# Kernel optimization log

Hardware: AMD Instinct MI355X
Metric: run time of the kernel (lower is better)

## Reference

```python
import jax, jax.numpy as jnp
import numpy as np
import math

B, S, E, H = 4, 1024, 1024, 16
D = E // H


def setup_inputs() -> dict:
    key = jax.random.key(0)
    ks = jax.random.split(key, 10)
    inp = {
        "query": jax.random.normal(ks[0], (B, S, E), dtype=jnp.float32),
        "key": jax.random.normal(ks[1], (B, S, E), dtype=jnp.float32),
        "value": jax.random.normal(ks[2], (B, S, E), dtype=jnp.float32),
        "attn_mask": jax.random.randint(ks[3], (B * H, S, S), 0, 2).astype(bool),
        "key_padding_mask": jax.random.randint(ks[4], (B, S), 0, 2).astype(bool),
        # nn.Linear(E, E, bias=False) weights, stored [out, in] as in torch
        "Wq": jax.random.normal(ks[5], (E, E), dtype=jnp.float32) * 0.02,
        "Wk": jax.random.normal(ks[6], (E, E), dtype=jnp.float32) * 0.02,
        "Wv": jax.random.normal(ks[7], (E, E), dtype=jnp.float32) * 0.02,
        "Wo": jax.random.normal(ks[8], (E, E), dtype=jnp.float32) * 0.02,
    }
    return inp


def reference(query, key, value, attn_mask, key_padding_mask, Wq, Wk, Wv, Wo):
    # projections: torch Linear => x @ W.T; split heads -> [B,H,S,D]
    Q = (query @ Wq.T).reshape(B, S, H, D).transpose(0, 2, 1, 3)
    K = (key @ Wk.T).reshape(B, S, H, D).transpose(0, 2, 1, 3)
    V = (value @ Wv.T).reshape(B, S, H, D).transpose(0, 2, 1, 3)

    scores = jnp.einsum('bhid,bhkd->bhik', Q, K) / math.sqrt(D)  # [B,H,S,S]

    am = attn_mask.reshape(B, H, S, S)
    kpm = jnp.broadcast_to(key_padding_mask[:, None, None, :], (B, H, S, S))
    mask = am | kpm

    # faithful quirks: masked scores set to 0 (not -inf); softmax over dim=2
    # (the QUERY axis i of [b,h,i,k]); masked weights zeroed after softmax.
    scores = jnp.where(mask, 0.0, scores)
    weights = jax.nn.softmax(scores, axis=2)
    weights = jnp.where(mask, 0.0, weights)

    attn = jnp.einsum('bhij,bhjk->bhik', weights, V)  # [B,H,S,D]
    attn = attn.transpose(0, 2, 1, 3).reshape(B, S, H * D)
    return attn @ Wo.T
```

## Files before the change

kernel.cpp:

```cpp
#include <hip/hip_runtime.h>
#include <stdint.h>

#define S_ 1024
#define E_ 1024
#define H_ 16
#define D_ 64
#define BH_ 64

typedef __attribute__((ext_vector_type(4))) float f32x4;
typedef __attribute__((ext_vector_type(8))) _Float16 f16x8;

__device__ __forceinline__ void gl_lds16(const void* g, void* l) {
  __builtin_amdgcn_global_load_lds((__attribute__((address_space(1))) void*)(g),
                                   (__attribute__((address_space(3))) void*)(l), 16, 0, 0);
}

__global__ __launch_bounds__(256) void cvt_f16(const float* __restrict__ q,
                                               const float* __restrict__ k,
                                               const float* __restrict__ v,
                                               const float* __restrict__ wq,
                                               const float* __restrict__ wk,
                                               const float* __restrict__ wv,
                                               const float* __restrict__ wo,
                                               _Float16* __restrict__ dst) {
  size_t i = ((size_t)blockIdx.x * 256 + threadIdx.x) * 4;
  const size_t M4 = 4u << 20, M1 = 1u << 20;
  const float* src;
  size_t off;
  if (i < M4) { src = q; off = i; }
  else if (i < 2 * M4) { src = k; off = i - M4; }
  else if (i < 3 * M4) { src = v; off = i - 2 * M4; }
  else if (i < 3 * M4 + M1) { src = wq; off = i - 3 * M4; }
  else if (i < 3 * M4 + 2 * M1) { src = wk; off = i - (3 * M4 + M1); }
  else if (i < 3 * M4 + 3 * M1) { src = wv; off = i - (3 * M4 + 2 * M1); }
  else { src = wo; off = i - (3 * M4 + 3 * M1); }
  float4 f = *reinterpret_cast<const float4*>(src + off);
  _Float16 h[4];
  h[0] = (_Float16)f.x; h[1] = (_Float16)f.y; h[2] = (_Float16)f.z; h[3] = (_Float16)f.w;
  *reinterpret_cast<uint2*>(dst + i) = *reinterpret_cast<uint2*>(h);
}

__global__ __launch_bounds__(256) void pack_mask(const int* __restrict__ am,
                                                 const int* __restrict__ kpm,
                                                 uint32_t* __restrict__ mw) {
  size_t t = (size_t)blockIdx.x * 256 + threadIdx.x;
  size_t f = t * 4;
  int k = (int)(f & (S_ - 1));
  int b = (int)(f >> 24);
  int4 a = *reinterpret_cast<const int4*>(am + f);
  int4 kp = *reinterpret_cast<const int4*>(kpm + (size_t)b * S_ + k);
  uint32_t nib = (uint32_t)((a.x | kp.x) != 0) | ((uint32_t)((a.y | kp.y) != 0) << 1) |
                 ((uint32_t)((a.z | kp.z) != 0) << 2) | ((uint32_t)((a.w | kp.w) != 0) << 3);
  uint32_t v = nib << ((threadIdx.x & 7) * 4);
  v |= __shfl_xor(v, 1);
  v |= __shfl_xor(v, 2);
  v |= __shfl_xor(v, 4);
  if ((threadIdx.x & 7) == 0) mw[t >> 3] = v;
}

__global__ __launch_bounds__(256) void gemm_proj(const _Float16* __restrict__ qkv,
                                                 const _Float16* __restrict__ wts,
                                                 _Float16* __restrict__ QKo,
                                                 _Float16* __restrict__ Vt) {
  const int K = 1024, BM = 128, BK = 32;
  __shared__ __align__(16) _Float16 As[BM * BK];
  __shared__ __align__(16) _Float16 Bs[BM * BK];
  const int tid = threadIdx.x, wave = tid >> 6, lane = tid & 63;
  const int l15 = lane & 15, lk = lane >> 4;
  const int wr = wave >> 1, wc = wave & 1;
  const int mb = blockIdx.x, nb = blockIdx.y, z = blockIdx.z;
  const _Float16* A = qkv + (size_t)z * (4u << 20);
  const _Float16* Bw = wts + (size_t)z * (1u << 20);
  const int srow = (lane >> 2);
  const int scol = (lane & 3) * 8;
  f32x4 acc[4][4] = {};
  for (int kt = 0; kt < K / BK; ++kt) {
#pragma unroll
    for (int c = 0; c < 2; ++c) {
      int ch = wave * 2 + c;
      int row = ch * 16 + srow;
      gl_lds16(&A[(size_t)(mb * BM + row) * K + kt * BK + scol], &As[ch * 512]);
      gl_lds16(&Bw[(size_t)(nb * BM + row) * K + kt * BK + scol], &Bs[ch * 512]);
    }
    __syncthreads();
    f16x8 a[4], b[4];
#pragma unroll
    for (int m = 0; m < 4; ++m)
      a[m] = *reinterpret_cast<const f16x8*>(&As[(wr * 64 + m * 16 + l15) * BK + lk * 8]);
#pragma unroll
    for (int n = 0; n < 4; ++n)
      b[n] = *reinterpret_cast<const f16x8*>(&Bs[(wc * 64 + n * 16 + l15) * BK + lk * 8]);
#pragma unroll
    for (int m = 0; m < 4; ++m)
#pragma unroll
      for (int n = 0; n < 4; ++n)
        acc[m][n] = __builtin_amdgcn_mfma_f32_16x16x32_f16(a[m], b[n], acc[m][n], 0, 0, 0);
    __syncthreads();
  }
  const float qs = (z == 0) ? 0.125f : 1.0f;
#pragma unroll
  for (int m = 0; m < 4; ++m) {
#pragma unroll
    for (int n = 0; n < 4; ++n) {
#pragma unroll
      for (int r = 0; r < 4; ++r) {
        int gm = mb * BM + wr * 64 + m * 16 + lk * 4 + r;
        int gn = nb * BM + wc * 64 + n * 16 + l15;
        int bb = gm >> 10, s = gm & 1023, h = gn >> 6, d = gn & 63;
        int bh = bb * 16 + h;
        _Float16 v = (_Float16)(acc[m][n][r] * qs);
        if (z == 2)
          Vt[((size_t)bh * D_ + d) * S_ + s] = v;
        else
          QKo[(size_t)z * (4u << 20) + ((size_t)bh * S_ + s) * D_ + d] = v;
      }
    }
  }
}

__global__ __launch_bounds__(256) void attn_pass_a(const _Float16* __restrict__ Qh,
                                                   const _Float16* __restrict__ Kh,
                                                   const uint32_t* __restrict__ mw,
                                                   float* __restrict__ denom,
                                                   _Float16* __restrict__ Wg) {
  const int TI = 128, TK = 128, LD = 72, LW = 144;
  __shared__ __align__(16) _Float16 Qs[TI * LD];
  __shared__ __align__(16) _Float16 Ks[TK * LD];
  __shared__ __align__(16) _Float16 Ws[TI * LW];
  __shared__ uint32_t Ms[TI * 4];
  __shared__ float red[4][64];
  const int tid = threadIdx.x, wave = tid >> 6, lane = tid & 63;
  const int l15 = lane & 15, lk = lane >> 4;
  const int wr = wave >> 1, wc = wave & 1;
  const int bh = blockIdx.y, kb = blockIdx.x;
  const _Float16* Qb = Qh + (size_t)bh * S_ * D_;
  const _Float16* Kb = Kh + (size_t)bh * S_ * D_;
  const uint32_t* mrow = mw + (size_t)bh * S_ * 32;
#pragma unroll
  for (int j = 0; j < 4; ++j) {
    int c = tid + j * 256;
    int row = c >> 3, c8 = c & 7;
    *reinterpret_cast<uint4*>(&Ks[row * LD + c8 * 8]) =
        *reinterpret_cast<const uint4*>(&Kb[(size_t)(kb * TK + row) * D_ + c8 * 8]);
  }
  float csum[4] = {0.f, 0.f, 0.f, 0.f};
  for (int ib = 0; ib < S_ / TI; ++ib) {
    __syncthreads();
#pragma unroll
    for (int j = 0; j < 4; ++j) {
      int c = tid + j * 256;
      int row = c >> 3, c8 = c & 7;
      *reinterpret_cast<uint4*>(&Qs[row * LD + c8 * 8]) =
          *reinterpret_cast<const uint4*>(&Qb[(size_t)(ib * TI + row) * D_ + c8 * 8]);
    }
    Ms[tid] = mrow[(size_t)(ib * TI + (tid >> 2)) * 32 + kb * 4 + (tid & 3)];
    Ms[tid + 256] = mrow[(size_t)(ib * TI + 64 + (tid >> 2)) * 32 + kb * 4 + (tid & 3)];
    __syncthreads();
    f32x4 acc[4][4] = {};
#pragma unroll
    for (int kk = 0; kk < 2; ++kk) {
      f16x8 a[4], b[4];
#pragma unroll
      for (int m = 0; m < 4; ++m)
        a[m] = *reinterpret_cast<const f16x8*>(&Qs[(wr * 64 + m * 16 + l15) * LD + kk * 32 + lk * 8]);
#pragma unroll
      for (int n = 0; n < 4; ++n)
        b[n] = *reinterpret_cast<const f16x8*>(&Ks[(wc * 64 + n * 16 + l15) * LD + kk * 32 + lk * 8]);
#pragma unroll
      for (int m = 0; m < 4; ++m)
#pragma unroll
        for (int n = 0; n < 4; ++n)
          acc[m][n] = __builtin_amdgcn_mfma_f32_16x16x32_f16(a[m], b[n], acc[m][n], 0, 0, 0);
    }
#pragma unroll
    for (int n = 0; n < 4; ++n) {
      int kcol = wc * 64 + n * 16 + l15;
      int kwl = kcol >> 5;
      int kbit = kcol & 31;
      float part = 0.f;
#pragma unroll
      for (int m = 0; m < 4; ++m) {
        int lr0 = wr * 64 + m * 16 + lk * 4;
#pragma unroll
        for (int r = 0; r < 4; ++r) {
          bool msk = (Ms[(lr0 + r) * 4 + kwl] >> kbit) & 1;
          float e = __expf(acc[m][n][r]);
          part += msk ? 1.0f : e;
          Ws[(lr0 + r) * LW + kcol] = msk ? (_Float16)0.f : (_Float16)e;
        }
      }
      csum[n] += part;
    }
    __syncthreads();
#pragma unroll
    for (int j = 0; j < 8; ++j) {
      int c = tid + j * 256;
      int row = c >> 4, col8 = c & 15;
      *reinterpret_cast<uint4*>(
          &Wg[((size_t)bh << 20) + (size_t)(ib * TI + row) * 1024 + kb * TK + col8 * 8]) =
          *reinterpret_cast<const uint4*>(&Ws[row * LW + col8 * 8]);
    }
  }
#pragma unroll
  for (int n = 0; n < 4; ++n) {
    float v = csum[n];
    v += __shfl_xor(v, 16);
    v += __shfl_xor(v, 32);
    csum[n] = v;
  }
  __syncthreads();
  if (lane < 16) {
#pragma unroll
    for (int n = 0; n < 4; ++n) red[wave][n * 16 + l15] = csum[n];
  }
  __syncthreads();
  if (tid < 128) {
    int wcx = tid >> 6, col = tid & 63;
    denom[(size_t)bh * S_ + kb * TK + wcx * 64 + col] = red[wcx][col] + red[wcx + 2][col];
  }
}

__global__ __launch_bounds__(256) void vscale(_Float16* __restrict__ Vt,
                                              const float* __restrict__ Dn) {
  size_t e = ((size_t)blockIdx.x * 256 + threadIdx.x) * 8;
  int bh = (int)(e >> 16);
  int s = (int)(e & (S_ - 1));
  uint4 raw = *reinterpret_cast<uint4*>(Vt + e);
  _Float16* h = reinterpret_cast<_Float16*>(&raw);
  const float* dp = Dn + (size_t)bh * S_ + s;
#pragma unroll
  for (int j = 0; j < 8; ++j) h[j] = (_Float16)((float)h[j] / dp[j]);
  *reinterpret_cast<uint4*>(Vt + e) = raw;
}

__global__ __launch_bounds__(256) void gemm_pv(const _Float16* __restrict__ Wg,
                                               const _Float16* __restrict__ Vp,
                                               _Float16* __restrict__ An) {
  const int BK = 64;
  __shared__ __align__(16) _Float16 As[128 * BK];
  __shared__ __align__(16) _Float16 Bs[64 * BK];
  const int tid = threadIdx.x, wave = tid >> 6, lane = tid & 63;
  const int l15 = lane & 15, lk = lane >> 4;
  const int wr = wave >> 1, wc = wave & 1;
  const int ibl = blockIdx.x, bh = blockIdx.y;
  const _Float16* Wb = Wg + ((size_t)bh << 20) + (size_t)ibl * 128 * 1024;
  const _Float16* Vb = Vp + ((size_t)bh << 16);
  f32x4 acc[4][2] = {};
  for (int kt = 0; kt < 16; ++kt) {
#pragma unroll
    for (int j = 0; j < 4; ++j) {
      int c = tid + j * 256;
      int row = c >> 3, slot = c & 7;
      int gs = slot ^ (row & 7);
      gl_lds16(&Wb[(size_t)row * 1024 + kt * BK + gs * 8], &As[c * 8]);
    }
#pragma unroll
    for (int j = 0; j < 2; ++j) {
      int c = tid + j * 256;
      int row = c >> 3, slot = c & 7;
      int gs = slot ^ (row & 7);
      gl_lds16(&Vb[(size_t)row * 1024 + kt * BK + gs * 8], &Bs[c * 8]);
    }
    __syncthreads();
#pragma unroll
    for (int kk = 0; kk < 2; ++kk) {
      f16x8 a[4], b[2];
#pragma unroll
      for (int m = 0; m < 4; ++m) {
        int row = wr * 64 + m * 16 + l15;
        int slot = (kk * 4 + lk) ^ (row & 7);
        a[m] = *reinterpret_cast<const f16x8*>(&As[row * BK + slot * 8]);
      }
#pragma unroll
      for (int n = 0; n < 2; ++n) {
        int row = wc * 32 + n * 16 + l15;
        int slot = (kk * 4 + lk) ^ (row & 7);
        b[n] = *reinterpret_cast<const f16x8*>(&Bs[row * BK + slot * 8]);
      }
#pragma unroll
      for (int m = 0; m < 4; ++m)
#pragma unroll
        for (int n = 0; n < 2; ++n)
          acc[m][n] = __builtin_amdgcn_mfma_f32_16x16x32_f16(a[m], b[n], acc[m][n], 0, 0, 0);
    }
    __syncthreads();
  }
  const int b_ = bh >> 4, h = bh & 15;
#pragma unroll
  for (int m = 0; m < 4; ++m) {
#pragma unroll
    for (int n = 0; n < 2; ++n) {
#pragma unroll
      for (int r = 0; r < 4; ++r) {
        int i = ibl * 128 + wr * 64 + m * 16 + lk * 4 + r;
        int d = wc * 32 + n * 16 + l15;
        An[((size_t)(b_ * S_ + i)) * E_ + h * D_ + d] = (_Float16)acc[m][n][r];
      }
    }
  }
}

__global__ __launch_bounds__(256) void gemm_out(const _Float16* __restrict__ An,
                                               const _Float16* __restrict__ Bw,
                                               float* __restrict__ outp) {
  const int K = 1024, BM = 128, BN = 64, BK = 32;
  __shared__ __align__(16) _Float16 As[BM * BK];
  __shared__ __align__(16) _Float16 Bs[BN * BK];
  const int tid = threadIdx.x, wave = tid >> 6, lane = tid & 63;
  const int l15 = lane & 15, lk = lane >> 4;
  const int wr = wave >> 1, wc = wave & 1;
  const int mb = blockIdx.x, nb = blockIdx.y;
  const int srow = (lane >> 2), scol = (lane & 3) * 8;
  f32x4 acc[4][2] = {};
  for (int kt = 0; kt < K / BK; ++kt) {
#pragma unroll
    for (int c = 0; c < 2; ++c) {
      int ch = wave * 2 + c;
      int row = ch * 16 + srow;
      gl_lds16(&An[(size_t)(mb * BM + row) * K + kt * BK + scol], &As[ch * 512]);
    }
    {
      int row = wave * 16 + srow;
      gl_lds16(&Bw[(size_t)(nb * BN + row) * K + kt * BK + scol], &Bs[wave * 512]);
    }
    __syncthreads();
    f16x8 a[4], b[2];
#pragma unroll
    for (int m = 0; m < 4; ++m)
      a[m] = *reinterpret_cast<const f16x8*>(&As[(wr * 64 + m * 16 + l15) * BK + lk * 8]);
#pragma unroll
    for (int n = 0; n < 2; ++n)
      b[n] = *reinterpret_cast<const f16x8*>(&Bs[(wc * 32 + n * 16 + l15) * BK + lk * 8]);
#pragma unroll
    for (int m = 0; m < 4; ++m)
#pragma unroll
      for (int n = 0; n < 2; ++n)
        acc[m][n] = __builtin_amdgcn_mfma_f32_16x16x32_f16(a[m], b[n], acc[m][n], 0, 0, 0);
    __syncthreads();
  }
#pragma unroll
  for (int m = 0; m < 4; ++m) {
#pragma unroll
    for (int n = 0; n < 2; ++n) {
#pragma unroll
      for (int r = 0; r < 4; ++r) {
        int gm = mb * BM + wr * 64 + m * 16 + lk * 4 + r;
        int gn = nb * BN + wc * 32 + n * 16 + l15;
        outp[(size_t)gm * 1024 + gn] = acc[m][n][r];
      }
    }
  }
}

extern "C" void kernel_launch(void* const* d_in, const int* in_sizes, int n_in,
                              void* d_out, int out_size, void* d_ws, size_t ws_size,
                              hipStream_t stream) {
  const float* q = (const float*)d_in[0];
  const float* k = (const float*)d_in[1];
  const float* v = (const float*)d_in[2];
  const int* am = (const int*)d_in[3];
  const int* kpm = (const int*)d_in[4];
  const float* Wq = (const float*)d_in[5];
  const float* Wk = (const float*)d_in[6];
  const float* Wv = (const float*)d_in[7];
  const float* Wo = (const float*)d_in[8];
  float* out = (float*)d_out;

  _Float16* cvt = (_Float16*)d_ws;
  _Float16* qkv = cvt;
  _Float16* wts = cvt + (12u << 20);
  _Float16* wob = cvt + (15u << 20);
  uint8_t* ws = (uint8_t*)d_ws;
  _Float16* Qh = (_Float16*)(ws + (32ull << 20));
  _Float16* Kh = (_Float16*)(ws + (40ull << 20));
  _Float16* Vt = (_Float16*)(ws + (48ull << 20));
  uint32_t* MW = (uint32_t*)(ws + (56ull << 20));
  float* Dn = (float*)(ws + (64ull << 20));
  _Float16* Wg = (_Float16*)(ws + (80ull << 20));
  _Float16* An = qkv;

  cvt_f16<<<16384, 256, 0, stream>>>(q, k, v, Wq, Wk, Wv, Wo, cvt);
  pack_mask<<<65536, 256, 0, stream>>>(am, kpm, MW);
  gemm_proj<<<dim3(32, 8, 3), 256, 0, stream>>>(qkv, wts, Qh, Vt);
  attn_pass_a<<<dim3(8, 64), 256, 0, stream>>>(Qh, Kh, MW, Dn, Wg);
  vscale<<<2048, 256, 0, stream>>>(Vt, Dn);
  gemm_pv<<<dim3(8, 64), 256, 0, stream>>>(Wg, Vt, An);
  gemm_out<<<dim3(32, 16), 256, 0, stream>>>(An, wob, out);
}
```

Measured before the change: 567.1 us.

## Recompute QK^T in PV kernel instead of materializing weight matrix

```diff
diff --git a/kernel.cpp b/kernel.cpp
--- a/kernel.cpp
+++ b/kernel.cpp
@@ -118,15 +118,13 @@
   }
 }
 
-__global__ __launch_bounds__(256) void attn_pass_a(const _Float16* __restrict__ Qh,
-                                                   const _Float16* __restrict__ Kh,
-                                                   const uint32_t* __restrict__ mw,
-                                                   float* __restrict__ denom,
-                                                   _Float16* __restrict__ Wg) {
-  const int TI = 128, TK = 128, LD = 72, LW = 144;
+__global__ __launch_bounds__(256) void attn_denom(const _Float16* __restrict__ Qh,
+                                                  const _Float16* __restrict__ Kh,
+                                                  const uint32_t* __restrict__ mw,
+                                                  float* __restrict__ denom) {
+  const int TI = 128, TK = 128, LD = 72;
   __shared__ __align__(16) _Float16 Qs[TI * LD];
   __shared__ __align__(16) _Float16 Ks[TK * LD];
-  __shared__ __align__(16) _Float16 Ws[TI * LW];
   __shared__ uint32_t Ms[TI * 4];
   __shared__ float red[4][64];
   const int tid = threadIdx.x, wave = tid >> 6, lane = tid & 63;
@@ -186,19 +184,9 @@
           bool msk = (Ms[(lr0 + r) * 4 + kwl] >> kbit) & 1;
           float e = __expf(acc[m][n][r]);
           part += msk ? 1.0f : e;
-          Ws[(lr0 + r) * LW + kcol] = msk ? (_Float16)0.f : (_Float16)e;
         }
       }
       csum[n] += part;
-    }
-    __syncthreads();
-#pragma unroll
-    for (int j = 0; j < 8; ++j) {
-      int c = tid + j * 256;
-      int row = c >> 4, col8 = c & 15;
-      *reinterpret_cast<uint4*>(
-          &Wg[((size_t)bh << 20) + (size_t)(ib * TI + row) * 1024 + kb * TK + col8 * 8]) =
-          *reinterpret_cast<const uint4*>(&Ws[row * LW + col8 * 8]);
     }
   }
 #pragma unroll
@@ -233,57 +221,93 @@
   *reinterpret_cast<uint4*>(Vt + e) = raw;
 }
 
-__global__ __launch_bounds__(256) void gemm_pv(const _Float16* __restrict__ Wg,
+__global__ __launch_bounds__(256) void attn_pv(const _Float16* __restrict__ Qh,
+                                               const _Float16* __restrict__ Kh,
                                                const _Float16* __restrict__ Vp,
+                                               const uint32_t* __restrict__ mw,
                                                _Float16* __restrict__ An) {
-  const int BK = 64;
-  __shared__ __align__(16) _Float16 As[128 * BK];
-  __shared__ __align__(16) _Float16 Bs[64 * BK];
+  const int TI = 128, TK = 128, LD = 72, LW = 136;
+  __shared__ __align__(16) _Float16 Qs[TI * LD];
+  __shared__ __align__(16) _Float16 Ks[TK * LD];
+  __shared__ __align__(16) _Float16 Ws[TI * LW];
+  __shared__ uint32_t Ms[TI * 4];
   const int tid = threadIdx.x, wave = tid >> 6, lane = tid & 63;
   const int l15 = lane & 15, lk = lane >> 4;
   const int wr = wave >> 1, wc = wave & 1;
-  const int ibl = blockIdx.x, bh = blockIdx.y;
-  const _Float16* Wb = Wg + ((size_t)bh << 20) + (size_t)ibl * 128 * 1024;
+  const int bh = blockIdx.y, ib = blockIdx.x;
+  const _Float16* Qb = Qh + (size_t)bh * S_ * D_;
+  const _Float16* Kb = Kh + (size_t)bh * S_ * D_;
   const _Float16* Vb = Vp + ((size_t)bh << 16);
-  f32x4 acc[4][2] = {};
-  for (int kt = 0; kt < 16; ++kt) {
+  const uint32_t* mrow = mw + (size_t)bh * S_ * 32;
+#pragma unroll
+  for (int j = 0; j < 4; ++j) {
+    int c = tid + j * 256;
+    int row = c >> 3, c8 = c & 7;
+    *reinterpret_cast<uint4*>(&Qs[row * LD + c8 * 8]) =
+        *reinterpret_cast<const uint4*>(&Qb[(size_t)(ib * TI + row) * D_ + c8 * 8]);
+  }
+  f32x4 acc2[4][2] = {};
+  for (int kt = 0; kt < S_ / TK; ++kt) {
+    __syncthreads();
 #pragma unroll
     for (int j = 0; j < 4; ++j) {
       int c = tid + j * 256;
-      int row = c >> 3, slot = c & 7;
-      int gs = slot ^ (row & 7);
-      gl_lds16(&Wb[(size_t)row * 1024 + kt * BK + gs * 8], &As[c * 8]);
-    }
-#pragma unroll
-    for (int j = 0; j < 2; ++j) {
-      int c = tid + j * 256;
-      int row = c >> 3, slot = c & 7;
-      int gs = slot ^ (row & 7);
-      gl_lds16(&Vb[(size_t)row * 1024 + kt * BK + gs * 8], &Bs[c * 8]);
-    }
-    __syncthreads();
+      int row = c >> 3, c8 = c & 7;
+      *reinterpret_cast<uint4*>(&Ks[row * LD + c8 * 8]) =
+          *reinterpret_cast<const uint4*>(&Kb[(size_t)(kt * TK + row) * D_ + c8 * 8]);
+    }
+    Ms[tid] = mrow[(size_t)(ib * TI + (tid >> 2)) * 32 + kt * 4 + (tid & 3)];
+    Ms[tid + 256] = mrow[(size_t)(ib * TI + 64 + (tid >> 2)) * 32 + kt * 4 + (tid & 3)];
+    __syncthreads();
+    f32x4 acc[4][4] = {};
 #pragma unroll
     for (int kk = 0; kk < 2; ++kk) {
-      f16x8 a[4], b[2];
+      f16x8 a[4], b[4];
+#pragma unroll
+      for (int m = 0; m < 4; ++m)
+        a[m] = *reinterpret_cast<const f16x8*>(&Qs[(wr * 64 + m * 16 + l15) * LD + kk * 32 + lk * 8]);
+#pragma unroll
+      for (int n = 0; n < 4; ++n)
+        b[n] = *reinterpret_cast<const f16x8*>(&Ks[(wc * 64 + n * 16 + l15) * LD + kk * 32 + lk * 8]);
+#pragma unroll
+      for (int m = 0; m < 4; ++m)
+#pragma unroll
+        for (int n = 0; n < 4; ++n)
+          acc[m][n] = __builtin_amdgcn_mfma_f32_16x16x32_f16(a[m], b[n], acc[m][n], 0, 0, 0);
+    }
+#pragma unroll
+    for (int n = 0; n < 4; ++n) {
+      int kcol = wc * 64 + n * 16 + l15;
+      int kwl = kcol >> 5;
+      int kbit = kcol & 31;
 #pragma unroll
       for (int m = 0; m < 4; ++m) {
-        int row = wr * 64 + m * 16 + l15;
-        int slot = (kk * 4 + lk) ^ (row & 7);
-        a[m] = *reinterpret_cast<const f16x8*>(&As[row * BK + slot * 8]);
+        int lr0 = wr * 64 + m * 16 + lk * 4;
+#pragma unroll
+        for (int r = 0; r < 4; ++r) {
+          bool msk = (Ms[(lr0 + r) * 4 + kwl] >> kbit) & 1;
+          float e = __expf(acc[m][n][r]);
+          Ws[(lr0 + r) * LW + kcol] = msk ? (_Float16)0.f : (_Float16)e;
+        }
       }
-#pragma unroll
-      for (int n = 0; n < 2; ++n) {
-        int row = wc * 32 + n * 16 + l15;
-        int slot = (kk * 4 + lk) ^ (row & 7);
-        b[n] = *reinterpret_cast<const f16x8*>(&Bs[row * BK + slot * 8]);
-      }
+    }
+    __syncthreads();
+#pragma unroll
+    for (int kk = 0; kk < 4; ++kk) {
+      f16x8 a2[4], b2[2];
+#pragma unroll
+      for (int m = 0; m < 4; ++m)
+        a2[m] = *reinterpret_cast<const f16x8*>(&Ws[(wr * 64 + m * 16 + l15) * LW + kk * 32 + lk * 8]);
+#pragma unroll
+      for (int n = 0; n < 2; ++n)
+        b2[n] = *reinterpret_cast<const f16x8*>(
+            &Vb[(size_t)(wc * 32 + n * 16 + l15) * S_ + kt * TK + kk * 32 + lk * 8]);
 #pragma unroll
       for (int m = 0; m < 4; ++m)
 #pragma unroll
         for (int n = 0; n < 2; ++n)
-          acc[m][n] = __builtin_amdgcn_mfma_f32_16x16x32_f16(a[m], b[n], acc[m][n], 0, 0, 0);
-    }
-    __syncthreads();
+          acc2[m][n] = __builtin_amdgcn_mfma_f32_16x16x32_f16(a2[m], b2[n], acc2[m][n], 0, 0, 0);
+    }
   }
   const int b_ = bh >> 4, h = bh & 15;
 #pragma unroll
@@ -292,9 +316,9 @@
     for (int n = 0; n < 2; ++n) {
 #pragma unroll
       for (int r = 0; r < 4; ++r) {
-        int i = ibl * 128 + wr * 64 + m * 16 + lk * 4 + r;
+        int i = ib * TI + wr * 64 + m * 16 + lk * 4 + r;
         int d = wc * 32 + n * 16 + l15;
-        An[((size_t)(b_ * S_ + i)) * E_ + h * D_ + d] = (_Float16)acc[m][n][r];
+        An[((size_t)(b_ * S_ + i)) * E_ + h * D_ + d] = (_Float16)acc2[m][n][r];
       }
     }
   }
@@ -376,14 +400,13 @@
   _Float16* Vt = (_Float16*)(ws + (48ull << 20));
   uint32_t* MW = (uint32_t*)(ws + (56ull << 20));
   float* Dn = (float*)(ws + (64ull << 20));
-  _Float16* Wg = (_Float16*)(ws + (80ull << 20));
   _Float16* An = qkv;
 
   cvt_f16<<<16384, 256, 0, stream>>>(q, k, v, Wq, Wk, Wv, Wo, cvt);
   pack_mask<<<65536, 256, 0, stream>>>(am, kpm, MW);
   gemm_proj<<<dim3(32, 8, 3), 256, 0, stream>>>(qkv, wts, Qh, Vt);
-  attn_pass_a<<<dim3(8, 64), 256, 0, stream>>>(Qh, Kh, MW, Dn, Wg);
+  attn_denom<<<dim3(8, 64), 256, 0, stream>>>(Qh, Kh, MW, Dn);
   vscale<<<2048, 256, 0, stream>>>(Vt, Dn);
-  gemm_pv<<<dim3(8, 64), 256, 0, stream>>>(Wg, Vt, An);
+  attn_pv<<<dim3(8, 64), 256, 0, stream>>>(Qh, Kh, Vt, MW, An);
   gemm_out<<<dim3(32, 16), 256, 0, stream>>>(An, wob, out);
 }
```

New measurement: 565.4 us. Within noise of the previous version (-0.3%).
